# Performance work log

Hardware: AMD Instinct MI355X
Metric: run time of the kernel (lower is better)

## Reference

```python
import jax, jax.numpy as jnp
import numpy as np

N_NODES = 50000
N_EDGES = 500000
NODE_DIM = 128
EDGE_DIM = 128
EPS = 1e-5


def layer_norm(x, gamma, beta):
    mu = jnp.mean(x, axis=-1, keepdims=True)
    var = jnp.var(x, axis=-1, keepdims=True)
    return (x - mu) * jax.lax.rsqrt(var + EPS) * gamma + beta


def setup_inputs() -> dict:
    key = jax.random.key(0)
    k = jax.random.split(key, 6)
    x = jax.random.normal(k[0], (N_NODES, NODE_DIM), dtype=jnp.float32)
    edge_index = jax.random.randint(k[1], (2, N_EDGES), 0, N_NODES, dtype=jnp.int32)
    edge_attr = jax.random.normal(k[2], (N_EDGES, EDGE_DIM), dtype=jnp.float32)
    in_dim = NODE_DIM * 2 + EDGE_DIM
    out_dim = EDGE_DIM * 2
    # Kaiming-uniform-ish init like torch.nn.Linear default
    lim = 1.0 / np.sqrt(in_dim)
    W = jax.random.uniform(k[3], (in_dim, out_dim), jnp.float32, -lim, lim)
    b = jax.random.uniform(k[4], (out_dim,), jnp.float32, -lim, lim)
    node_gamma = jnp.ones((NODE_DIM,), jnp.float32)
    node_beta = jnp.zeros((NODE_DIM,), jnp.float32)
    edge_gamma = jnp.ones((EDGE_DIM,), jnp.float32)
    edge_beta = jnp.zeros((EDGE_DIM,), jnp.float32)
    return {
        "x": x,
        "edge_index": edge_index,
        "edge_attr": edge_attr,
        "W": W,
        "b": b,
        "node_gamma": node_gamma,
        "node_beta": node_beta,
        "edge_gamma": edge_gamma,
        "edge_beta": edge_beta,
    }


def reference(x, edge_index, edge_attr, W, b, node_gamma, node_beta, edge_gamma, edge_beta):
    src = edge_index[0]
    dst = edge_index[1]
    # per-node LayerNorm over feature dim (PGLayerNorm mode='node')
    xn = layer_norm(x, node_gamma, node_beta)                 # [N, D]
    m = jnp.concatenate([xn[src], xn[dst], edge_attr], axis=-1)  # [E, 2D+De]
    raw = jax.nn.relu(m @ W + b)                               # [E, 2*De]
    delta, gate_logit = jnp.split(raw, 2, axis=-1)
    out = edge_attr + jax.nn.sigmoid(gate_logit) * delta       # gated residual
    return layer_norm(out, edge_gamma, edge_beta)
```

## Files before the change

kernel.cpp:

```cpp
#include <hip/hip_runtime.h>
#include <hip/hip_bf16.h>

#define N_NODES 50000
#define N_EDGES 500000
#define D 128
#define OUTD 256

typedef float f32x4 __attribute__((ext_vector_type(4)));
typedef unsigned int u32x4 __attribute__((ext_vector_type(4)));
typedef __bf16 bf16x8 __attribute__((ext_vector_type(8)));

__device__ __forceinline__ unsigned short f2bf(float x) {
    unsigned u = __float_as_uint(x);
    unsigned r = (u + 0x7fffu + ((u >> 16) & 1u)) >> 16;
    return (unsigned short)r;
}

__global__ __launch_bounds__(256) void node_ln(
    const float* __restrict__ x, const float* __restrict__ gamma,
    const float* __restrict__ beta, unsigned short* __restrict__ xn)
{
    int w = threadIdx.x >> 6, lane = threadIdx.x & 63;
    int row = blockIdx.x * 4 + w;
    const float2 v = *(const float2*)(x + (size_t)row * D + lane * 2);
    float s = v.x + v.y;
    float q = v.x * v.x + v.y * v.y;
#pragma unroll
    for (int m = 1; m < 64; m <<= 1) {
        s += __shfl_xor(s, m, 64);
        q += __shfl_xor(q, m, 64);
    }
    float mean = s * (1.f / 128.f);
    float var = q * (1.f / 128.f) - mean * mean;
    float rs = rsqrtf(var + 1e-5f);
    float2 gg = *(const float2*)(gamma + lane * 2);
    float2 bb = *(const float2*)(beta + lane * 2);
    float y0 = (v.x - mean) * rs * gg.x + bb.x;
    float y1 = (v.y - mean) * rs * gg.y + bb.y;
    unsigned int pack = (unsigned)f2bf(y0) | ((unsigned)f2bf(y1) << 16);
    *(unsigned int*)(xn + (size_t)row * D + lane * 2) = pack;
}

__global__ __launch_bounds__(256) void repack_w(
    const float* __restrict__ W, unsigned short* __restrict__ Wp)
{
    int tid = blockIdx.x * 256 + threadIdx.x;
    int k = tid >> 8;
    int col = tid & 255;
    float v = W[tid];
    int dst = (k >> 3) * 2048 + col * 8 + (k & 7);
    Wp[dst] = f2bf(v);
}

__global__ __launch_bounds__(512) void edge_kernel(
    const unsigned short* __restrict__ xn, const unsigned short* __restrict__ Wp,
    const int* __restrict__ eidx, const float* __restrict__ ea,
    const float* __restrict__ bias, const float* __restrict__ egamma,
    const float* __restrict__ ebeta, float* __restrict__ out)
{
    __shared__ unsigned short A_lds[128 * 128];
    __shared__ unsigned short B_lds[32768];
    __shared__ float red_s[128 * 4];
    __shared__ float red_q[128 * 4];

    const int t = threadIdx.x;
    const int lane = t & 63;
    const int w = t >> 6;
    const int wm = w >> 2, wn = w & 3;
    const int lhi = lane >> 4, llo = lane & 15;
    const int e0 = blockIdx.x * 128;

    f32x4 acc[4][4];
#pragma unroll
    for (int a = 0; a < 4; ++a)
#pragma unroll
        for (int b2 = 0; b2 < 4; ++b2)
            acc[a][b2] = f32x4{0.f, 0.f, 0.f, 0.f};

    const int srow = t >> 2;
    const int sq4 = t & 3;
    const int se = (e0 + srow < N_EDGES) ? (e0 + srow) : (N_EDGES - 1);

    for (int chunk = 0; chunk < 3; ++chunk) {
        if (chunk < 2) {
            const int node = eidx[chunk * N_EDGES + se];
            const u32x4* src = (const u32x4*)(xn + (size_t)node * D);
#pragma unroll
            for (int c = 0; c < 4; ++c) {
                int q16 = sq4 * 4 + c;
                u32x4 v = src[q16];
                *(u32x4*)((char*)A_lds + srow * 256 + ((q16 ^ (srow & 7)) << 4)) = v;
            }
        } else {
            const float* src = ea + (size_t)se * D;
#pragma unroll
            for (int c = 0; c < 4; ++c) {
                int q16 = sq4 * 4 + c;
                f32x4 v0 = *(const f32x4*)(src + q16 * 8);
                f32x4 v1 = *(const f32x4*)(src + q16 * 8 + 4);
                u32x4 p;
                p.x = (unsigned)f2bf(v0.x) | ((unsigned)f2bf(v0.y) << 16);
                p.y = (unsigned)f2bf(v0.z) | ((unsigned)f2bf(v0.w) << 16);
                p.z = (unsigned)f2bf(v1.x) | ((unsigned)f2bf(v1.y) << 16);
                p.w = (unsigned)f2bf(v1.z) | ((unsigned)f2bf(v1.w) << 16);
                *(u32x4*)((char*)A_lds + srow * 256 + ((q16 ^ (srow & 7)) << 4)) = p;
            }
        }
        {
            const u32x4* wp = (const u32x4*)(Wp + chunk * 32768);
#pragma unroll
            for (int i = 0; i < 8; ++i) {
                int idx = i * 512 + t;
                *(u32x4*)((char*)B_lds + idx * 16) = wp[idx];
            }
        }
        __syncthreads();
#pragma unroll
        for (int kq = 0; kq < 4; ++kq) {
            bf16x8 af[4], bfr[4];
#pragma unroll
            for (int mt = 0; mt < 4; ++mt) {
                int row = wm * 64 + mt * 16 + llo;
                int slot = (kq * 4 + lhi) ^ (row & 7);
                af[mt] = *(const bf16x8*)((char*)A_lds + row * 256 + (slot << 4));
            }
#pragma unroll
            for (int nt = 0; nt < 4; ++nt) {
                int colb = (nt < 2) ? (wn * 32 + nt * 16)
                                    : (128 + wn * 32 + (nt - 2) * 16);
                int col = colb + llo;
                bfr[nt] = *(const bf16x8*)((char*)B_lds + ((kq * 4 + lhi) * 256 + col) * 16);
            }
#pragma unroll
            for (int mt = 0; mt < 4; ++mt)
#pragma unroll
                for (int nt = 0; nt < 4; ++nt)
                    acc[mt][nt] = __builtin_amdgcn_mfma_f32_16x16x32_bf16(
                        af[mt], bfr[nt], acc[mt][nt], 0, 0, 0);
        }
        __syncthreads();
    }

    const int c0 = wn * 32 + llo;
    const int c1 = c0 + 16;
    const float b_d0 = bias[c0], b_d1 = bias[c1];
    const float b_g0 = bias[128 + c0], b_g1 = bias[128 + c1];
    const float g0 = egamma[c0], g1 = egamma[c1];
    const float be0 = ebeta[c0], be1 = ebeta[c1];

    float o0[4][4], o1[4][4];
#pragma unroll
    for (int mt = 0; mt < 4; ++mt) {
#pragma unroll
        for (int i = 0; i < 4; ++i) {
            int rl = wm * 64 + mt * 16 + lhi * 4 + i;
            int e = e0 + rl;
            int ecl = (e < N_EDGES) ? e : (N_EDGES - 1);
            float rd0 = fmaxf(acc[mt][0][i] + b_d0, 0.f);
            float rd1 = fmaxf(acc[mt][1][i] + b_d1, 0.f);
            float rg0 = fmaxf(acc[mt][2][i] + b_g0, 0.f);
            float rg1 = fmaxf(acc[mt][3][i] + b_g1, 0.f);
            float ea0 = ea[(size_t)ecl * D + c0];
            float ea1 = ea[(size_t)ecl * D + c1];
            float v0 = ea0 + rd0 / (1.f + __expf(-rg0));
            float v1 = ea1 + rd1 / (1.f + __expf(-rg1));
            o0[mt][i] = v0;
            o1[mt][i] = v1;
            float s = v0 + v1, q = v0 * v0 + v1 * v1;
#pragma unroll
            for (int m = 1; m < 16; m <<= 1) {
                s += __shfl_xor(s, m, 64);
                q += __shfl_xor(q, m, 64);
            }
            if (llo == 0) {
                red_s[rl * 4 + wn] = s;
                red_q[rl * 4 + wn] = q;
            }
        }
    }
    __syncthreads();
#pragma unroll
    for (int mt = 0; mt < 4; ++mt) {
#pragma unroll
        for (int i = 0; i < 4; ++i) {
            int rl = wm * 64 + mt * 16 + lhi * 4 + i;
            int e = e0 + rl;
            float s = red_s[rl * 4 + 0] + red_s[rl * 4 + 1] +
                      red_s[rl * 4 + 2] + red_s[rl * 4 + 3];
            float q = red_q[rl * 4 + 0] + red_q[rl * 4 + 1] +
                      red_q[rl * 4 + 2] + red_q[rl * 4 + 3];
            float mean = s * (1.f / 128.f);
            float var = q * (1.f / 128.f) - mean * mean;
            float rs = rsqrtf(var + 1e-5f);
            float y0 = (o0[mt][i] - mean) * rs * g0 + be0;
            float y1 = (o1[mt][i] - mean) * rs * g1 + be1;
            if (e < N_EDGES) {
                out[(size_t)e * D + c0] = y0;
                out[(size_t)e * D + c1] = y1;
            }
        }
    }
}

extern "C" void kernel_launch(void* const* d_in, const int* in_sizes, int n_in,
                              void* d_out, int out_size, void* d_ws, size_t ws_size,
                              hipStream_t stream)
{
    const float* x = (const float*)d_in[0];
    const int* eidx = (const int*)d_in[1];
    const float* ea = (const float*)d_in[2];
    const float* W = (const float*)d_in[3];
    const float* b = (const float*)d_in[4];
    const float* ngamma = (const float*)d_in[5];
    const float* nbeta = (const float*)d_in[6];
    const float* egamma = (const float*)d_in[7];
    const float* ebeta = (const float*)d_in[8];
    float* out = (float*)d_out;

    unsigned short* xn = (unsigned short*)d_ws;
    unsigned short* Wp = xn + (size_t)N_NODES * D;

    node_ln<<<N_NODES / 4, 256, 0, stream>>>(x, ngamma, nbeta, xn);
    repack_w<<<384, 256, 0, stream>>>(W, Wp);
    edge_kernel<<<(N_EDGES + 127) / 128, 512, 0, stream>>>(
        xn, Wp, eidx, ea, b, egamma, ebeta, out);
}
```

Measured before the change: 669.5 us.

## Gather node rows via direct-to-LDS loads, read W from global, drop B tile

Node-feature gathers for the source and destination chunks now use global_load_lds, which writes straight into the swizzled A tile without a register round trip. The B tile in shared memory is gone; each wave reads its W fragments directly from global memory, relying on L1/L2 caching. This cuts shared memory per block from about 100KB to about 36KB, and the launch bound now asks for 4 blocks per CU to raise occupancy. The residual edge_attr in the epilogue is read back as bf16 from the LDS tile instead of as fp32 from global, which saves traffic but loses precision in the residual.

```diff
diff --git a/kernel.cpp b/kernel.cpp
--- a/kernel.cpp
+++ b/kernel.cpp
@@ -14,6 +14,13 @@
     unsigned u = __float_as_uint(x);
     unsigned r = (u + 0x7fffu + ((u >> 16) & 1u)) >> 16;
     return (unsigned short)r;
+}
+
+__device__ __forceinline__ void gload_lds16(const void* g, void* l) {
+    __builtin_amdgcn_global_load_lds(
+        (const __attribute__((address_space(1))) unsigned int*)g,
+        (__attribute__((address_space(3))) unsigned int*)l,
+        16, 0, 0);
 }
 
 __global__ __launch_bounds__(256) void node_ln(
@@ -52,14 +59,13 @@
     Wp[dst] = f2bf(v);
 }
 
-__global__ __launch_bounds__(512) void edge_kernel(
+__global__ __launch_bounds__(512, 4) void edge_kernel(
     const unsigned short* __restrict__ xn, const unsigned short* __restrict__ Wp,
     const int* __restrict__ eidx, const float* __restrict__ ea,
     const float* __restrict__ bias, const float* __restrict__ egamma,
     const float* __restrict__ ebeta, float* __restrict__ out)
 {
-    __shared__ unsigned short A_lds[128 * 128];
-    __shared__ unsigned short B_lds[32768];
+    __shared__ __align__(16) unsigned short A_lds[128 * 128];
     __shared__ float red_s[128 * 4];
     __shared__ float red_q[128 * 4];
 
@@ -83,13 +89,16 @@
 
     for (int chunk = 0; chunk < 3; ++chunk) {
         if (chunk < 2) {
-            const int node = eidx[chunk * N_EDGES + se];
-            const u32x4* src = (const u32x4*)(xn + (size_t)node * D);
+            const int rb = w * 16;
 #pragma unroll
             for (int c = 0; c < 4; ++c) {
-                int q16 = sq4 * 4 + c;
-                u32x4 v = src[q16];
-                *(u32x4*)((char*)A_lds + srow * 256 + ((q16 ^ (srow & 7)) << 4)) = v;
+                const int rloc = rb + c * 4 + lhi;
+                const int e = e0 + rloc;
+                const int ecl = (e < N_EDGES) ? e : (N_EDGES - 1);
+                const int node = eidx[chunk * N_EDGES + ecl];
+                const char* src = (const char*)(xn + (size_t)node * D)
+                                + ((llo ^ (rloc & 7)) << 4);
+                gload_lds16(src, (char*)A_lds + (rb + c * 4) * 256);
             }
         } else {
             const float* src = ea + (size_t)se * D;
@@ -106,30 +115,23 @@
                 *(u32x4*)((char*)A_lds + srow * 256 + ((q16 ^ (srow & 7)) << 4)) = p;
             }
         }
-        {
-            const u32x4* wp = (const u32x4*)(Wp + chunk * 32768);
-#pragma unroll
-            for (int i = 0; i < 8; ++i) {
-                int idx = i * 512 + t;
-                *(u32x4*)((char*)B_lds + idx * 16) = wp[idx];
-            }
-        }
         __syncthreads();
+        const unsigned short* wb = Wp + (size_t)chunk * 32768;
 #pragma unroll
         for (int kq = 0; kq < 4; ++kq) {
             bf16x8 af[4], bfr[4];
+#pragma unroll
+            for (int nt = 0; nt < 4; ++nt) {
+                int colb = (nt < 2) ? (wn * 32 + nt * 16)
+                                    : (128 + wn * 32 + (nt - 2) * 16);
+                bfr[nt] = *(const bf16x8*)(wb + (kq * 4 + lhi) * 2048
+                                              + (colb + llo) * 8);
+            }
 #pragma unroll
             for (int mt = 0; mt < 4; ++mt) {
                 int row = wm * 64 + mt * 16 + llo;
                 int slot = (kq * 4 + lhi) ^ (row & 7);
                 af[mt] = *(const bf16x8*)((char*)A_lds + row * 256 + (slot << 4));
-            }
-#pragma unroll
-            for (int nt = 0; nt < 4; ++nt) {
-                int colb = (nt < 2) ? (wn * 32 + nt * 16)
-                                    : (128 + wn * 32 + (nt - 2) * 16);
-                int col = colb + llo;
-                bfr[nt] = *(const bf16x8*)((char*)B_lds + ((kq * 4 + lhi) * 256 + col) * 16);
             }
 #pragma unroll
             for (int mt = 0; mt < 4; ++mt)
@@ -147,6 +149,8 @@
     const float b_g0 = bias[128 + c0], b_g1 = bias[128 + c1];
     const float g0 = egamma[c0], g1 = egamma[c1];
     const float be0 = ebeta[c0], be1 = ebeta[c1];
+    const int q0 = c0 >> 3, q1 = c1 >> 3;
+    const int o0b = (c0 & 7) * 2, o1b = (c1 & 7) * 2;
 
     float o0[4][4], o1[4][4];
 #pragma unroll
@@ -154,14 +158,16 @@
 #pragma unroll
         for (int i = 0; i < 4; ++i) {
             int rl = wm * 64 + mt * 16 + lhi * 4 + i;
-            int e = e0 + rl;
-            int ecl = (e < N_EDGES) ? e : (N_EDGES - 1);
             float rd0 = fmaxf(acc[mt][0][i] + b_d0, 0.f);
             float rd1 = fmaxf(acc[mt][1][i] + b_d1, 0.f);
             float rg0 = fmaxf(acc[mt][2][i] + b_g0, 0.f);
             float rg1 = fmaxf(acc[mt][3][i] + b_g1, 0.f);
-            float ea0 = ea[(size_t)ecl * D + c0];
-            float ea1 = ea[(size_t)ecl * D + c1];
+            unsigned short u0 = *(const unsigned short*)((const char*)A_lds
+                + rl * 256 + ((q0 ^ (rl & 7)) << 4) + o0b);
+            unsigned short u1 = *(const unsigned short*)((const char*)A_lds
+                + rl * 256 + ((q1 ^ (rl & 7)) << 4) + o1b);
+            float ea0 = __uint_as_float((unsigned)u0 << 16);
+            float ea1 = __uint_as_float((unsigned)u1 << 16);
             float v0 = ea0 + rd0 / (1.f + __expf(-rg0));
             float v1 = ea1 + rd1 / (1.f + __expf(-rg1));
             o0[mt][i] = v0;
```

Result: faster. 596.1 us (-11.0%).
